# Kernel tuning notes

Measured on AMD Instinct MI355X. Metric: run time of the kernel, lower is better.

## Reference

```python
import jax, jax.numpy as jnp
import numpy as np

D_MODEL, D_EDGE, D_STRUCT = 128, 64, 8
N, E, B = 50000, 800000, 1

def _lin(key, din, dout):
    kw, kb = jax.random.split(key)
    s = 1.0 / np.sqrt(din)
    return (jax.random.uniform(kw, (din, dout), jnp.float32, -s, s),
            jax.random.uniform(kb, (dout,), jnp.float32, -s, s))

def setup_inputs() -> dict:
    key = jax.random.key(0)
    ks = jax.random.split(key, 16)
    H = jax.random.normal(ks[0], (B, N, D_MODEL), jnp.float32)
    xyz = jax.random.normal(ks[1], (B, N, 3), jnp.float32)
    edge_index = jax.random.randint(ks[2], (2, E), 0, N, jnp.int64)
    edge_struct = jax.random.normal(ks[3], (E, D_STRUCT), jnp.float32)
    edge_rest_lengths = jax.random.uniform(ks[4], (E,), jnp.float32)
    We1, be1 = _lin(ks[5], 2 * D_MODEL + 2 + D_STRUCT, D_EDGE)
    We2, be2 = _lin(ks[6], D_EDGE, D_EDGE)
    Wg1, bg1 = _lin(ks[7], 2 + D_STRUCT, 32)
    Wg2, bg2 = _lin(ks[8], 32, 1)
    Wn1, bn1 = _lin(ks[9], D_MODEL + D_EDGE, 2 * D_MODEL)
    Wn2, bn2 = _lin(ks[10], 2 * D_MODEL, D_MODEL)
    ln_g = jnp.ones((D_MODEL,), jnp.float32)
    ln_b = jnp.zeros((D_MODEL,), jnp.float32)
    return dict(H=H, xyz=xyz, edge_index=edge_index, edge_struct=edge_struct,
                edge_rest_lengths=edge_rest_lengths,
                We1=We1, be1=be1, We2=We2, be2=be2,
                Wg1=Wg1, bg1=bg1, Wg2=Wg2, bg2=bg2,
                Wn1=Wn1, bn1=bn1, Wn2=Wn2, bn2=bn2,
                ln_g=ln_g, ln_b=ln_b)

def reference(H, xyz, edge_index, edge_struct, edge_rest_lengths,
              We1, be1, We2, be2, Wg1, bg1, Wg2, bg2,
              Wn1, bn1, Wn2, bn2, ln_g, ln_b):
    Bn, Nn, d = H.shape
    i, j = edge_index[0], edge_index[1]
    # edge geometry
    diff = xyz[:, i, :] - xyz[:, j, :]                      # (B,E,3)
    dist2 = jnp.sum(diff * diff, axis=-1, keepdims=True)    # (B,E,1)
    dist = jnp.sqrt(dist2 + 1e-9)
    rest = edge_rest_lengths.reshape(1, -1, 1)
    delta = (dist - rest) / (rest + 1e-9)
    struct = jnp.broadcast_to(edge_struct[None], (Bn, edge_struct.shape[0], edge_struct.shape[1]))
    # edge message MLP
    Hi, Hj = H[:, i, :], H[:, j, :]
    e_in = jnp.concatenate([Hi, Hj, dist2, delta, struct], axis=-1)  # (B,E,2d+2+ds)
    e = jax.nn.silu(e_in @ We1 + be1)
    e_msg = jax.nn.silu(e @ We2 + be2)                       # (B,E,d_edge)
    # gate
    g_in = jnp.concatenate([dist2, delta, struct], axis=-1)
    g = jax.nn.sigmoid(jax.nn.silu(g_in @ Wg1 + bg1) @ Wg2 + bg2)  # (B,E,1)
    e_msg = e_msg * g
    # scatter-add aggregate to destination node i
    agg = jnp.zeros((Bn, Nn, e_msg.shape[-1]), H.dtype).at[:, i, :].add(e_msg)
    # node MLP (dropout is identity at eval) + residual + LayerNorm
    n_in = jnp.concatenate([H, agg], axis=-1)
    upd = jax.nn.silu(n_in @ Wn1 + bn1) @ Wn2 + bn2
    x = H + upd
    mu = jnp.mean(x, axis=-1, keepdims=True)
    var = jnp.mean((x - mu) ** 2, axis=-1, keepdims=True)
    return (x - mu) / jnp.sqrt(var + 1e-5) * ln_g + ln_b
```

## Files before the change

kernel.cpp:

```cpp
#include <hip/hip_runtime.h>
#include <stdint.h>

#define N_NODES 50000
#define N_EDGES 800000
#define NODE_TILES 782

#define SE   72
#define SW2  72
#define SPQ  136
#define SN1  216
#define SN2  280
#define ATS  40
#define MSTR 72

#define EC_GRID 962
#define EC_CHUNK 13

#define SCAN_B 98

#define FP_PQ_BLOCKS 256
#define FP_GRID 2048
#define FP_FILL_STRIDE ((FP_GRID - FP_PQ_BLOCKS) * 256)

typedef short bf16x8 __attribute__((ext_vector_type(8)));
typedef short short4v __attribute__((ext_vector_type(4)));
typedef unsigned short ushort8 __attribute__((ext_vector_type(8)));
typedef float f32x4  __attribute__((ext_vector_type(4)));

static __device__ __forceinline__ unsigned short f2bf(float f) {
  unsigned int x = __float_as_uint(f);
  unsigned int r = (x + 0x7fffu + ((x >> 16) & 1u)) >> 16;
  return (unsigned short)r;
}
static __device__ __forceinline__ float bf2f(unsigned short u) {
  return __uint_as_float(((unsigned int)u) << 16);
}
static __device__ __forceinline__ float silu_f(float x) {
  return x * __builtin_amdgcn_rcpf(1.0f + __expf(-x));
}
static __device__ __forceinline__ float sigmoid_f(float x) {
  return __builtin_amdgcn_rcpf(1.0f + __expf(-x));
}
static __device__ __forceinline__ unsigned int cvt_pk_bf16(float lo, float hi) {
  unsigned int r;
  asm("v_cvt_pk_bf16_f32 %0, %1, %2" : "=v"(r) : "v"(lo), "v"(hi));
  return r;
}
static __device__ __forceinline__ bf16x8 pack8(float4 u, float4 v) {
  bf16x8 w;
  w[0] = (short)f2bf(u.x); w[1] = (short)f2bf(u.y);
  w[2] = (short)f2bf(u.z); w[3] = (short)f2bf(u.w);
  w[4] = (short)f2bf(v.x); w[5] = (short)f2bf(v.y);
  w[6] = (short)f2bf(v.z); w[7] = (short)f2bf(v.w);
  return w;
}

__global__ void prep_hist(
    const int* __restrict__ eidx,
    const float* __restrict__ We1, const float* __restrict__ be1,
    const float* __restrict__ We2,
    const float* __restrict__ Wn1, const float* __restrict__ Wn2,
    unsigned short* __restrict__ WpqT, unsigned short* __restrict__ We2T,
    unsigned short* __restrict__ Wn1T, unsigned short* __restrict__ Wn2T,
    unsigned short* __restrict__ WrT,
    int* __restrict__ cnt)
{
  const int gid = blockIdx.x * 256 + threadIdx.x;
  const int gsz = gridDim.x * 256;
  for (int i = gid; i < 128 * SPQ; i += gsz) {
    int n = i / SPQ, k = i % SPQ;
    unsigned short v = 0;
    if (k < 128) v = (n < 64) ? f2bf(We1[k * 64 + n]) : f2bf(We1[(128 + k) * 64 + (n - 64)]);
    WpqT[i] = v;
  }
  for (int i = gid; i < 64 * SW2; i += gsz) {
    int n = i / SW2, k = i % SW2;
    We2T[i] = (k < 64) ? f2bf(We2[k * 64 + n]) : (unsigned short)0;
  }
  for (int i = gid; i < 256 * SN1; i += gsz) {
    int n = i / SN1, k = i % SN1;
    Wn1T[i] = (k < 192) ? f2bf(Wn1[k * 256 + n]) : (unsigned short)0;
  }
  for (int i = gid; i < 128 * SN2; i += gsz) {
    int n = i / SN2, k = i % SN2;
    Wn2T[i] = (k < 256) ? f2bf(Wn2[k * 128 + n]) : (unsigned short)0;
  }
  for (int i = gid; i < 64 * 32; i += gsz) {
    int n = i >> 5, k = i & 31;
    float v = 0.f;
    if (k < 2)       v = We1[256 * 64 + n];
    else if (k < 4)  v = We1[257 * 64 + n];
    else if (k < 12) v = We1[(258 + (k - 4)) * 64 + n];
    else if (k == 12) v = be1[n];
    else if (k == 13) { float w = We1[256 * 64 + n]; v = w - bf2f(f2bf(w)); }
    else if (k == 14) { float w = We1[257 * 64 + n]; v = w - bf2f(f2bf(w)); }
    else if (k == 15) { float w = be1[n];            v = w - bf2f(f2bf(w)); }
    WrT[i] = (k < 16) ? f2bf(v) : (unsigned short)0;
  }
  if (gid < N_EDGES) atomicAdd(&cnt[eidx[gid]], 1);
}

__global__ __launch_bounds__(512) void scan_local(
    const int* __restrict__ cnt, int* __restrict__ rowptr,
    int* __restrict__ bsum)
{
  __shared__ int wsum[8], woff[8];
  const int t = threadIdx.x;
  const int idx = blockIdx.x * 512 + t;
  const int lane = t & 63, wid = t >> 6;
  int c = (idx < N_NODES) ? cnt[idx] : 0;
  int v = c;
  #pragma unroll
  for (int o = 1; o < 64; o <<= 1) {
    int u = __shfl_up(v, o);
    if (lane >= o) v += u;
  }
  if (lane == 63) wsum[wid] = v;
  __syncthreads();
  if (t == 0) {
    int a = 0;
    #pragma unroll
    for (int w = 0; w < 8; ++w) { woff[w] = a; a += wsum[w]; }
    bsum[blockIdx.x] = a;
  }
  __syncthreads();
  if (idx < N_NODES) rowptr[idx] = woff[wid] + (v - c);
}

__global__ __launch_bounds__(128) void scan_mid(
    const int* __restrict__ bsum, int* __restrict__ boff)
{
  __shared__ int ws[2];
  const int t = threadIdx.x;
  const int lane = t & 63, wid = t >> 6;
  int c = (t < SCAN_B) ? bsum[t] : 0;
  int v = c;
  #pragma unroll
  for (int o = 1; o < 64; o <<= 1) {
    int u = __shfl_up(v, o);
    if (lane >= o) v += u;
  }
  if (lane == 63) ws[wid] = v;
  __syncthreads();
  int add = (wid == 1) ? ws[0] : 0;
  if (t < SCAN_B) boff[t] = add + (v - c);
}

__global__ __launch_bounds__(512) void scan_add(
    const int* __restrict__ rowptr, const int* __restrict__ boff,
    int* __restrict__ cursor, float4* __restrict__ agg)
{
  const int idx = blockIdx.x * 512 + threadIdx.x;
  if (idx < N_NODES) cursor[idx] = rowptr[idx] + boff[blockIdx.x];
  if (idx < 50048) {
    float4 z = make_float4(0.f, 0.f, 0.f, 0.f);
    float4* p = agg + (long)idx * 16;
    #pragma unroll
    for (int k = 0; k < 16; ++k) p[k] = z;
  }
}

__global__ __launch_bounds__(256, 3) void fill_pq(
    const float* __restrict__ H, const unsigned short* __restrict__ WpqT,
    unsigned short* __restrict__ P, unsigned short* __restrict__ Q,
    unsigned short* __restrict__ Hbf,
    const int* __restrict__ eidx, const float* __restrict__ xyz,
    const float* __restrict__ estruct, const float* __restrict__ erest,
    int* __restrict__ cursor,
    const float* __restrict__ Wg1, const float* __restrict__ bg1,
    const float* __restrict__ Wg2, const float* __restrict__ bg2,
    unsigned short* __restrict__ rec)
{
  __shared__ unsigned short As[64 * SPQ];
  __shared__ unsigned short Ws[128 * SPQ];

  const int bid = blockIdx.x;
  const int tid = threadIdx.x;

  if (bid < FP_PQ_BLOCKS) {
    const int lane = tid & 63;
    const int wv   = tid >> 6;
    const int lr   = lane & 15;
    const int lq   = lane >> 4;
    const int m0   = wv * 16;

    for (int i = tid * 8; i < 128 * SPQ; i += 256 * 8)
      *(bf16x8*)&Ws[i] = *(const bf16x8*)&WpqT[i];

    f32x4 zero4 = {0.f, 0.f, 0.f, 0.f};
    for (int t = bid; t < NODE_TILES; t += FP_PQ_BLOCKS) {
      const int n0 = t * 64;
      __syncthreads();
      {
        int le = tid >> 2, q = tid & 3;
        int node = n0 + le; if (node >= N_NODES) node = N_NODES - 1;
        const float* src = H + (long)node * 128 + q * 32;
        unsigned short* dst = &As[le * SPQ + q * 32];
        #pragma unroll
        for (int c = 0; c < 32; c += 8) {
          float4 u = *(const float4*)(src + c);
          float4 v = *(const float4*)(src + c + 4);
          *(bf16x8*)(dst + c) = pack8(u, v);
        }
      }
      __syncthreads();

      for (int idx = tid * 8; idx < 64 * 128; idx += 256 * 8) {
        int row = idx >> 7, col = idx & 127;
        *(bf16x8*)&Hbf[((long)n0 + row) * 128 + col] = *(const bf16x8*)&As[row * SPQ + col];
      }

      f32x4 acc[8];
      #pragma unroll
      for (int f = 0; f < 8; ++f) acc[f] = zero4;
      #pragma unroll
      for (int s = 0; s < 4; ++s) {
        int kb = s * 32 + lq * 8;
        bf16x8 a = *(const bf16x8*)&As[(m0 + lr) * SPQ + kb];
        #pragma unroll
        for (int f = 0; f < 8; ++f) {
          bf16x8 b = *(const bf16x8*)&Ws[(f * 16 + lr) * SPQ + kb];
          acc[f] = __builtin_amdgcn_mfma_f32_16x16x32_bf16(a, b, acc[f], 0, 0, 0);
        }
      }
      #pragma unroll
      for (int f = 0; f < 8; ++f) {
        #pragma unroll
        for (int r = 0; r < 4; ++r) {
          int node = n0 + m0 + lq * 4 + r;
          if (node < N_NODES) {
            if (f < 4) P[(long)node * 64 + f * 16 + lr] = f2bf(acc[f][r]);
            else       Q[(long)node * 64 + (f - 4) * 16 + lr] = f2bf(acc[f][r]);
          }
        }
      }
    }
  } else {
    for (int e = (bid - FP_PQ_BLOCKS) * 256 + tid; e < N_EDGES; e += FP_FILL_STRIDE) {
      int i = eidx[e], j = eidx[N_EDGES + e];
      float dx = xyz[i * 3 + 0] - xyz[j * 3 + 0];
      float dy = xyz[i * 3 + 1] - xyz[j * 3 + 1];
      float dz = xyz[i * 3 + 2] - xyz[j * 3 + 2];
      float d2 = dx * dx + dy * dy + dz * dz;
      float dist = sqrtf(d2 + 1e-9f);
      float rest = erest[e];
      float dl = (dist - rest) / (rest + 1e-9f);
      float4 s0 = *(const float4*)&estruct[e * 8];
      float4 s1 = *(const float4*)&estruct[e * 8 + 4];
      float st[8] = {s0.x, s0.y, s0.z, s0.w, s1.x, s1.y, s1.z, s1.w};
      float gsum = 0.f;
      #pragma unroll
      for (int h = 0; h < 32; ++h) {
        float a = bg1[h] + d2 * Wg1[0 * 32 + h] + dl * Wg1[1 * 32 + h];
        #pragma unroll
        for (int c = 0; c < 8; ++c) a += st[c] * Wg1[(2 + c) * 32 + h];
        gsum += silu_f(a) * Wg2[h];
      }
      float g = sigmoid_f(gsum + bg2[0]);

      unsigned short d2h = f2bf(d2);
      unsigned short d2l = f2bf(d2 - bf2f(d2h));
      unsigned short dlh = f2bf(dl);
      unsigned short dll = f2bf(dl - bf2f(dlh));

      ushort8 w0;
      w0[0] = d2h; w0[1] = d2l; w0[2] = dlh; w0[3] = dll;
      w0[4] = f2bf(st[0]); w0[5] = f2bf(st[1]); w0[6] = f2bf(st[2]); w0[7] = f2bf(st[3]);
      uint4 w1;
      w1.x = (unsigned int)f2bf(st[4]) | ((unsigned int)f2bf(st[5]) << 16);
      w1.y = (unsigned int)f2bf(st[6]) | ((unsigned int)f2bf(st[7]) << 16);
      w1.z = __float_as_uint(g);
      w1.w = (unsigned int)i | ((unsigned int)j << 16);

      int pos = atomicAdd(&cursor[i], 1);
      unsigned short* dst = rec + (long)pos * 16;
      *(ushort8*)dst = w0;
      *(uint4*)(dst + 8) = w1;
    }
  }
}

__global__ __launch_bounds__(256, 4) void edge_compute(
    const unsigned short* __restrict__ P, const unsigned short* __restrict__ Q,
    const unsigned short* __restrict__ rec,
    const unsigned short* __restrict__ We2T, const float* __restrict__ be2,
    const unsigned short* __restrict__ WrT,
    float* __restrict__ agg)
{
  __shared__ unsigned short W2s[64 * SW2];
  __shared__ unsigned short Es [4 * 16 * SE];
  __shared__ unsigned short At [4 * 16 * ATS];
  __shared__ unsigned short Ms [4 * 16 * MSTR];

  const int tid  = threadIdx.x;
  const int lane = tid & 63;
  const int wv   = tid >> 6;
  const int lr   = lane & 15;
  const int lq   = lane >> 4;

  for (int i = tid * 8; i < 64 * SW2; i += 256 * 8)
    *(bf16x8*)&W2s[i] = *(const bf16x8*)&We2T[i];

  unsigned short* Es_w = &Es[wv * 16 * SE];
  unsigned short* At_w = &At[wv * 16 * ATS];
  unsigned short* Ms_w = &Ms[wv * 16 * MSTR];

  if (lane < 16) {
    ushort8 z;
    #pragma unroll
    for (int c = 0; c < 8; ++c) z[c] = 0;
    *(ushort8*)&At_w[lane * ATS + 16] = z;
    *(ushort8*)&At_w[lane * ATS + 24] = z;
  }

  bf16x8 aWr[4];
  float bias2[4][4];
  #pragma unroll
  for (int f = 0; f < 4; ++f) {
    aWr[f] = *(const bf16x8*)&WrT[(f * 16 + lr) * 32 + lq * 8];
    #pragma unroll
    for (int r = 0; r < 4; ++r) bias2[f][r] = be2[f * 16 + lq * 4 + r];
  }
  __syncthreads();

  const int n_tiles = N_EDGES / 16;
  const int wid = blockIdx.x * 4 + wv;
  const int t0 = wid * EC_CHUNK;
  const int t1 = (t0 + EC_CHUNK < n_tiles) ? (t0 + EC_CHUNK) : n_tiles;
  if (t0 >= n_tiles) return;

  f32x4 zero4 = {0.f, 0.f, 0.f, 0.f};
  int   cur_node;
  {
    int ij0 = *(const int*)(rec + (long)t0 * 16 * 16 + 14);
    cur_node = ij0 & 0xffff;
  }
  float acc        = 0.f;
  bool  use_atomic = true;

  for (int tile = t0; tile < t1; ++tile) {
    const int s0 = tile * 16;

    const unsigned short* rp = rec + (long)(s0 + lr) * 16;
    ushort8 ra = *(const ushort8*)rp;
    uint4   rb = *(const uint4*)(rp + 8);
    float g     = __uint_as_float(rb.z);
    int   inode = (int)(rb.w & 0xffff);
    int   jnode = (int)((rb.w >> 16) & 0xffff);

    if (lane < 16) {
      ushort8 w1;
      w1[0] = (unsigned short)(rb.x & 0xffff);
      w1[1] = (unsigned short)(rb.x >> 16);
      w1[2] = (unsigned short)(rb.y & 0xffff);
      w1[3] = (unsigned short)(rb.y >> 16);
      w1[4] = 0x3F80u; w1[5] = (unsigned short)ra[0];
      w1[6] = (unsigned short)ra[2]; w1[7] = 0x3F80u;
      *(ushort8*)&At_w[lane * ATS]     = ra;
      *(ushort8*)&At_w[lane * ATS + 8] = w1;
    }

    bf16x8 bA = *(const bf16x8*)&At_w[lr * ATS + lq * 8];
    f32x4 acc1[4];
    #pragma unroll
    for (int f = 0; f < 4; ++f)
      acc1[f] = __builtin_amdgcn_mfma_f32_16x16x32_bf16(aWr[f], bA, zero4, 0, 0, 0);

    const unsigned short* Pb = P + (long)inode * 64;
    const unsigned short* Qb = Q + (long)jnode * 64;
    #pragma unroll
    for (int f = 0; f < 4; ++f) {
      short4v pv = *(const short4v*)&Pb[f * 16 + lq * 4];
      short4v qv = *(const short4v*)&Qb[f * 16 + lq * 4];
      float v0 = silu_f(bf2f((unsigned short)pv[0]) + bf2f((unsigned short)qv[0]) + acc1[f][0]);
      float v1 = silu_f(bf2f((unsigned short)pv[1]) + bf2f((unsigned short)qv[1]) + acc1[f][1]);
      float v2 = silu_f(bf2f((unsigned short)pv[2]) + bf2f((unsigned short)qv[2]) + acc1[f][2]);
      float v3 = silu_f(bf2f((unsigned short)pv[3]) + bf2f((unsigned short)qv[3]) + acc1[f][3]);
      uint2 w;
      w.x = cvt_pk_bf16(v0, v1);
      w.y = cvt_pk_bf16(v2, v3);
      *(uint2*)&Es_w[lr * SE + f * 16 + lq * 4] = w;
    }

    f32x4 acc2[4];
    #pragma unroll
    for (int f = 0; f < 4; ++f) acc2[f] = zero4;
    #pragma unroll
    for (int s = 0; s < 2; ++s) {
      int kb = s * 32 + lq * 8;
      bf16x8 bE = *(const bf16x8*)&Es_w[lr * SE + kb];
      #pragma unroll
      for (int f = 0; f < 4; ++f) {
        bf16x8 aW = *(const bf16x8*)&W2s[(f * 16 + lr) * SW2 + kb];
        acc2[f] = __builtin_amdgcn_mfma_f32_16x16x32_bf16(aW, bE, acc2[f], 0, 0, 0);
      }
    }

    #pragma unroll
    for (int f = 0; f < 4; ++f) {
      float o0 = silu_f(acc2[f][0] + bias2[f][0]) * g;
      float o1 = silu_f(acc2[f][1] + bias2[f][1]) * g;
      float o2 = silu_f(acc2[f][2] + bias2[f][2]) * g;
      float o3 = silu_f(acc2[f][3] + bias2[f][3]) * g;
      uint2 w;
      w.x = cvt_pk_bf16(o0, o1);
      w.y = cvt_pk_bf16(o2, o3);
      *(uint2*)&Ms_w[lr * MSTR + f * 16 + lq * 4] = w;
    }

    float mv[16];
    #pragma unroll
    for (int e = 0; e < 16; ++e) mv[e] = bf2f(Ms_w[e * MSTR + lane]);

    int up = __shfl_up(inode, 1);
    unsigned long long bm = __ballot(inode != up);
    unsigned mask = (unsigned)bm & 0xFFFEu;
    int i0 = __builtin_amdgcn_readlane(inode, 0);
    if (i0 != cur_node) mask |= 1u;

    #pragma unroll
    for (int e = 0; e < 16; ++e) {
      if (mask & (1u << e)) {
        if (use_atomic) atomicAdd(&agg[(long)cur_node * 64 + lane], acc);
        else            agg[(long)cur_node * 64 + lane] = acc;
        use_atomic = false;
        cur_node = __builtin_amdgcn_readlane(inode, e);
        acc = 0.f;
      }
      acc += mv[e];
    }
  }
  atomicAdd(&agg[(long)cur_node * 64 + lane], acc);
}

__global__ __launch_bounds__(256, 2) void h1_kernel(
    const unsigned short* __restrict__ Hbf, const float* __restrict__ agg,
    const unsigned short* __restrict__ Wn1T, const float* __restrict__ bn1,
    unsigned short* __restrict__ h1)
{
  __shared__ unsigned short Wl[128 * SN1];

  const int tid  = threadIdx.x;
  const int lane = tid & 63;
  const int wv   = tid >> 6;
  const int lr   = lane & 15;
  const int lq   = lane >> 4;
  const int m0   = wv * 16;
  const int p    = blockIdx.x & 1;

  for (int i = tid * 8; i < 128 * SN1; i += 256 * 8)
    *(bf16x8*)&Wl[i] = *(const bf16x8*)&Wn1T[p * 128 * SN1 + i];
  __syncthreads();

  f32x4 zero4 = {0.f, 0.f, 0.f, 0.f};
  for (int t = blockIdx.x >> 1; t < NODE_TILES; t += 256) {
    const int n0 = t * 64;
    int rowa = n0 + m0 + lr;
    int rowc = rowa < N_NODES ? rowa : N_NODES - 1;

    f32x4 acc1[8];
    #pragma unroll
    for (int f = 0; f < 8; ++f) acc1[f] = zero4;
    #pragma unroll
    for (int s = 0; s < 6; ++s) {
      int kb = s * 32 + lq * 8;
      bf16x8 a;
      if (s < 4) {
        a = *(const bf16x8*)&Hbf[(long)rowa * 128 + kb];
      } else {
        const float* pp = agg + (long)rowc * 64 + (kb - 128);
        float4 u = *(const float4*)pp;
        float4 v = *(const float4*)(pp + 4);
        a = pack8(u, v);
      }
      #pragma unroll
      for (int f = 0; f < 8; ++f) {
        bf16x8 b = *(const bf16x8*)&Wl[(f * 16 + lr) * SN1 + kb];
        acc1[f] = __builtin_amdgcn_mfma_f32_16x16x32_bf16(a, b, acc1[f], 0, 0, 0);
      }
    }
    #pragma unroll
    for (int f = 0; f < 8; ++f) {
      int col = p * 128 + f * 16 + lr;
      float bias = bn1[col];
      #pragma unroll
      for (int r = 0; r < 4; ++r) {
        int node = n0 + m0 + lq * 4 + r;
        h1[(long)node * 256 + col] = f2bf(silu_f(acc1[f][r] + bias));
      }
    }
  }
}

__global__ __launch_bounds__(256, 2) void out_kernel(
    const float* __restrict__ H, const unsigned short* __restrict__ h1,
    const unsigned short* __restrict__ Wn2T, const float* __restrict__ bn2,
    const float* __restrict__ ln_g, const float* __restrict__ ln_b,
    float* __restrict__ out)
{
  __shared__ unsigned short Wl[128 * SN2];

  const int tid  = threadIdx.x;
  const int lane = tid & 63;
  const int wv   = tid >> 6;
  const int lr   = lane & 15;
  const int lq   = lane >> 4;
  const int m0   = wv * 16;

  for (int i = tid * 8; i < 128 * SN2; i += 256 * 8)
    *(bf16x8*)&Wl[i] = *(const bf16x8*)&Wn2T[i];
  __syncthreads();

  f32x4 zero4 = {0.f, 0.f, 0.f, 0.f};
  for (int t = blockIdx.x; t < NODE_TILES; t += 512) {
    const int n0 = t * 64;
    int rowa = n0 + m0 + lr;

    f32x4 acc2[8];
    #pragma unroll
    for (int f = 0; f < 8; ++f) acc2[f] = zero4;
    #pragma unroll
    for (int s = 0; s < 8; ++s) {
      int kb = s * 32 + lq * 8;
      bf16x8 a = *(const bf16x8*)&h1[(long)rowa * 256 + kb];
      #pragma unroll
      for (int f = 0; f < 8; ++f) {
        bf16x8 b = *(const bf16x8*)&Wl[(f * 16 + lr) * SN2 + kb];
        acc2[f] = __builtin_amdgcn_mfma_f32_16x16x32_bf16(a, b, acc2[f], 0, 0, 0);
      }
    }

    #pragma unroll
    for (int r = 0; r < 4; ++r) {
      int node = n0 + m0 + lq * 4 + r;
      int nc = node < N_NODES ? node : N_NODES - 1;
      float x[8];
      float sum = 0.f, sumsq = 0.f;
      #pragma unroll
      for (int f = 0; f < 8; ++f) {
        int n = f * 16 + lr;
        float u = acc2[f][r] + bn2[n];
        float xv = H[(long)nc * 128 + n] + u;
        x[f] = xv;
        sum += xv;
        sumsq += xv * xv;
      }
      #pragma unroll
      for (int o = 1; o < 16; o <<= 1) {
        sum   += __shfl_xor(sum, o);
        sumsq += __shfl_xor(sumsq, o);
      }
      float mu  = sum * (1.f / 128.f);
      float var = sumsq * (1.f / 128.f) - mu * mu;
      float rstd = rsqrtf(var + 1e-5f);
      if (node < N_NODES) {
        #pragma unroll
        for (int f = 0; f < 8; ++f) {
          int n = f * 16 + lr;
          out[(long)node * 128 + n] = (x[f] - mu) * rstd * ln_g[n] + ln_b[n];
        }
      }
    }
  }
}

extern "C" void kernel_launch(void* const* d_in, const int* in_sizes, int n_in,
                              void* d_out, int out_size, void* d_ws, size_t ws_size,
                              hipStream_t stream) {
  const float* H       = (const float*)d_in[0];
  const float* xyz     = (const float*)d_in[1];
  const int*   eidx    = (const int*)d_in[2];
  const float* estruct = (const float*)d_in[3];
  const float* erest   = (const float*)d_in[4];
  const float* We1     = (const float*)d_in[5];
  const float* be1     = (const float*)d_in[6];
  const float* We2     = (const float*)d_in[7];
  const float* be2     = (const float*)d_in[8];
  const float* Wg1     = (const float*)d_in[9];
  const float* bg1     = (const float*)d_in[10];
  const float* Wg2     = (const float*)d_in[11];
  const float* bg2     = (const float*)d_in[12];
  const float* Wn1     = (const float*)d_in[13];
  const float* bn1     = (const float*)d_in[14];
  const float* Wn2     = (const float*)d_in[15];
  const float* bn2     = (const float*)d_in[16];
  const float* ln_g    = (const float*)d_in[17];
  const float* ln_b    = (const float*)d_in[18];

  char* ws = (char*)d_ws;
  float*          agg    = (float*)(ws + 0);
  unsigned short* Hbf    = (unsigned short*)(ws + 12812288);
  unsigned short* rec    = (unsigned short*)(ws + 25624576);
  unsigned short* P      = (unsigned short*)(ws + 51224576);
  unsigned short* Qm     = (unsigned short*)(ws + 57624576);
  int*            cnt    = (int*)(ws + 64024576);
  int*            rowptr = (int*)(ws + 64224768);
  int*            cursor = (int*)(ws + 64424960);
  unsigned short* WpqT   = (unsigned short*)(ws + 64625152);
  unsigned short* We2T   = (unsigned short*)(ws + 64659968);
  unsigned short* Wn1T   = (unsigned short*)(ws + 64669184);
  unsigned short* Wn2T   = (unsigned short*)(ws + 64779776);
  unsigned short* WrT    = (unsigned short*)(ws + 64851456);
  int*            bsum   = (int*)(ws + 64855552);
  int*            boff   = (int*)(ws + 64856064);
  unsigned short* h1     = (unsigned short*)(ws + 64856576);
  float* out = (float*)d_out;

  hipMemsetAsync(cnt, 0, (size_t)N_NODES * sizeof(int), stream);

  hipLaunchKernelGGL(prep_hist, dim3(3125), dim3(256), 0, stream,
                     eidx, We1, be1, We2, Wn1, Wn2, WpqT, We2T, Wn1T, Wn2T, WrT, cnt);
  hipLaunchKernelGGL(scan_local, dim3(SCAN_B), dim3(512), 0, stream,
                     cnt, rowptr, bsum);
  hipLaunchKernelGGL(scan_mid, dim3(1), dim3(128), 0, stream,
                     bsum, boff);
  hipLaunchKernelGGL(scan_add, dim3(SCAN_B), dim3(512), 0, stream,
                     rowptr, boff, cursor, (float4*)agg);
  hipLaunchKernelGGL(fill_pq, dim3(FP_GRID), dim3(256), 0, stream,
                     H, WpqT, P, Qm, Hbf,
                     eidx, xyz, estruct, erest, cursor,
                     Wg1, bg1, Wg2, bg2, rec);
  hipLaunchKernelGGL(edge_compute, dim3(EC_GRID), dim3(256), 0, stream,
                     P, Qm, rec, We2T, be2, WrT, agg);
  hipLaunchKernelGGL(h1_kernel, dim3(512), dim3(256), 0, stream,
                     Hbf, agg, Wn1T, bn1, h1);
  hipLaunchKernelGGL(out_kernel, dim3(512), dim3(256), 0, stream,
                     H, h1, Wn2T, bn2, ln_g, ln_b, out);
}
```

Before: 381.0 us.

## Split fill_pq work by wave instead of by block, load H directly to registers

Rather than dedicating whole blocks to either the node projection GEMM or the edge fill, every block now gives two waves a 64-node tile (each wave covering 32 rows) and the other two waves the edge loop. The As staging buffer and its syncs are removed: H rows are read from global memory, packed to bf16 in registers, written to Hbf and fed straight into the MFMAs. The grid shrinks to 1024 blocks and launch bounds allow 4 blocks per SM to raise occupancy. The aim is to overlap GEMM and edge work inside each CU and cut LDS traffic. In exchange, every block now loads the full weight tile into LDS, and the global H reads are less coalesced.

```diff
diff --git a/kernel.cpp b/kernel.cpp
--- a/kernel.cpp
+++ b/kernel.cpp
@@ -18,9 +18,7 @@
 
 #define SCAN_B 98
 
-#define FP_PQ_BLOCKS 256
-#define FP_GRID 2048
-#define FP_FILL_STRIDE ((FP_GRID - FP_PQ_BLOCKS) * 256)
+#define FP_GRID 1024
 
 typedef short bf16x8 __attribute__((ext_vector_type(8)));
 typedef short short4v __attribute__((ext_vector_type(4)));
@@ -160,7 +158,7 @@
   }
 }
 
-__global__ __launch_bounds__(256, 3) void fill_pq(
+__global__ __launch_bounds__(256, 4) void fill_pq(
     const float* __restrict__ H, const unsigned short* __restrict__ WpqT,
     unsigned short* __restrict__ P, unsigned short* __restrict__ Q,
     unsigned short* __restrict__ Hbf,
@@ -171,72 +169,67 @@
     const float* __restrict__ Wg2, const float* __restrict__ bg2,
     unsigned short* __restrict__ rec)
 {
-  __shared__ unsigned short As[64 * SPQ];
   __shared__ unsigned short Ws[128 * SPQ];
 
   const int bid = blockIdx.x;
   const int tid = threadIdx.x;
-
-  if (bid < FP_PQ_BLOCKS) {
-    const int lane = tid & 63;
-    const int wv   = tid >> 6;
-    const int lr   = lane & 15;
-    const int lq   = lane >> 4;
-    const int m0   = wv * 16;
-
-    for (int i = tid * 8; i < 128 * SPQ; i += 256 * 8)
-      *(bf16x8*)&Ws[i] = *(const bf16x8*)&WpqT[i];
-
-    f32x4 zero4 = {0.f, 0.f, 0.f, 0.f};
-    for (int t = bid; t < NODE_TILES; t += FP_PQ_BLOCKS) {
-      const int n0 = t * 64;
-      __syncthreads();
-      {
-        int le = tid >> 2, q = tid & 3;
-        int node = n0 + le; if (node >= N_NODES) node = N_NODES - 1;
-        const float* src = H + (long)node * 128 + q * 32;
-        unsigned short* dst = &As[le * SPQ + q * 32];
+  const int wv  = tid >> 6;
+
+  for (int i = tid * 8; i < 128 * SPQ; i += 256 * 8)
+    *(bf16x8*)&Ws[i] = *(const bf16x8*)&WpqT[i];
+  __syncthreads();
+
+  if (wv < 2) {
+    if (bid < NODE_TILES) {
+      const int lane = tid & 63;
+      const int lr   = lane & 15;
+      const int lq   = lane >> 4;
+      const int n0   = bid * 64;
+      const int m0   = wv * 32;
+
+      f32x4 zero4 = {0.f, 0.f, 0.f, 0.f};
+      f32x4 acc[2][8];
+      #pragma unroll
+      for (int h = 0; h < 2; ++h)
         #pragma unroll
-        for (int c = 0; c < 32; c += 8) {
-          float4 u = *(const float4*)(src + c);
-          float4 v = *(const float4*)(src + c + 4);
-          *(bf16x8*)(dst + c) = pack8(u, v);
-        }
-      }
-      __syncthreads();
-
-      for (int idx = tid * 8; idx < 64 * 128; idx += 256 * 8) {
-        int row = idx >> 7, col = idx & 127;
-        *(bf16x8*)&Hbf[((long)n0 + row) * 128 + col] = *(const bf16x8*)&As[row * SPQ + col];
-      }
-
-      f32x4 acc[8];
-      #pragma unroll
-      for (int f = 0; f < 8; ++f) acc[f] = zero4;
+        for (int f = 0; f < 8; ++f) acc[h][f] = zero4;
+
       #pragma unroll
       for (int s = 0; s < 4; ++s) {
         int kb = s * 32 + lq * 8;
-        bf16x8 a = *(const bf16x8*)&As[(m0 + lr) * SPQ + kb];
+        #pragma unroll
+        for (int h = 0; h < 2; ++h) {
+          int rowa = n0 + m0 + h * 16 + lr;
+          int rowc = rowa < N_NODES ? rowa : N_NODES - 1;
+          const float* p = H + (long)rowc * 128 + kb;
+          float4 u = *(const float4*)p;
+          float4 v = *(const float4*)(p + 4);
+          bf16x8 a = pack8(u, v);
+          *(bf16x8*)&Hbf[(long)rowa * 128 + kb] = a;
+          #pragma unroll
+          for (int f = 0; f < 8; ++f) {
+            bf16x8 b = *(const bf16x8*)&Ws[(f * 16 + lr) * SPQ + kb];
+            acc[h][f] = __builtin_amdgcn_mfma_f32_16x16x32_bf16(a, b, acc[h][f], 0, 0, 0);
+          }
+        }
+      }
+      #pragma unroll
+      for (int h = 0; h < 2; ++h) {
         #pragma unroll
         for (int f = 0; f < 8; ++f) {
-          bf16x8 b = *(const bf16x8*)&Ws[(f * 16 + lr) * SPQ + kb];
-          acc[f] = __builtin_amdgcn_mfma_f32_16x16x32_bf16(a, b, acc[f], 0, 0, 0);
-        }
-      }
-      #pragma unroll
-      for (int f = 0; f < 8; ++f) {
-        #pragma unroll
-        for (int r = 0; r < 4; ++r) {
-          int node = n0 + m0 + lq * 4 + r;
-          if (node < N_NODES) {
-            if (f < 4) P[(long)node * 64 + f * 16 + lr] = f2bf(acc[f][r]);
-            else       Q[(long)node * 64 + (f - 4) * 16 + lr] = f2bf(acc[f][r]);
+          #pragma unroll
+          for (int r = 0; r < 4; ++r) {
+            int node = n0 + m0 + h * 16 + lq * 4 + r;
+            if (node < N_NODES) {
+              if (f < 4) P[(long)node * 64 + f * 16 + lr] = f2bf(acc[h][f][r]);
+              else       Q[(long)node * 64 + (f - 4) * 16 + lr] = f2bf(acc[h][f][r]);
+            }
           }
         }
       }
     }
   } else {
-    for (int e = (bid - FP_PQ_BLOCKS) * 256 + tid; e < N_EDGES; e += FP_FILL_STRIDE) {
+    for (int e = bid * 128 + (tid - 128); e < N_EDGES; e += FP_GRID * 128) {
       int i = eidx[e], j = eidx[N_EDGES + e];
       float dx = xyz[i * 3 + 0] - xyz[j * 3 + 0];
       float dy = xyz[i * 3 + 1] - xyz[j * 3 + 1];
```

Result: no change. 381.2 us (+0.0%).

## Split fused fill/PQ kernel into separate edge-fill and node-GEMM launches

Applied to the files above, without the earlier changes.

Replaces the block-specialized fill_pq kernel, which gave some blocks the node projection and the rest a grid-stride edge fill, with two kernels. One runs one thread per edge for geometry, gate and reorder, and the other runs one block per 64-node tile for the projection. The projection now loads H rows straight into registers as MFMA A operands instead of staging them through shared memory. This removes load imbalance and the shared-memory staging, but loses the overlap of the two phases and adds a kernel launch.

```diff
diff --git a/kernel.cpp b/kernel.cpp
--- a/kernel.cpp
+++ b/kernel.cpp
@@ -17,10 +17,6 @@
 #define EC_CHUNK 13
 
 #define SCAN_B 98
-
-#define FP_PQ_BLOCKS 256
-#define FP_GRID 2048
-#define FP_FILL_STRIDE ((FP_GRID - FP_PQ_BLOCKS) * 256)
 
 typedef short bf16x8 __attribute__((ext_vector_type(8)));
 typedef short short4v __attribute__((ext_vector_type(4)));
@@ -160,10 +156,7 @@
   }
 }
 
-__global__ __launch_bounds__(256, 3) void fill_pq(
-    const float* __restrict__ H, const unsigned short* __restrict__ WpqT,
-    unsigned short* __restrict__ P, unsigned short* __restrict__ Q,
-    unsigned short* __restrict__ Hbf,
+__global__ void fill_reorder(
     const int* __restrict__ eidx, const float* __restrict__ xyz,
     const float* __restrict__ estruct, const float* __restrict__ erest,
     int* __restrict__ cursor,
@@ -171,111 +164,99 @@
     const float* __restrict__ Wg2, const float* __restrict__ bg2,
     unsigned short* __restrict__ rec)
 {
-  __shared__ unsigned short As[64 * SPQ];
+  int e = blockIdx.x * 256 + threadIdx.x;
+  if (e >= N_EDGES) return;
+  int i = eidx[e], j = eidx[N_EDGES + e];
+  float dx = xyz[i * 3 + 0] - xyz[j * 3 + 0];
+  float dy = xyz[i * 3 + 1] - xyz[j * 3 + 1];
+  float dz = xyz[i * 3 + 2] - xyz[j * 3 + 2];
+  float d2 = dx * dx + dy * dy + dz * dz;
+  float dist = sqrtf(d2 + 1e-9f);
+  float rest = erest[e];
+  float dl = (dist - rest) / (rest + 1e-9f);
+  float4 s0 = *(const float4*)&estruct[e * 8];
+  float4 s1 = *(const float4*)&estruct[e * 8 + 4];
+  float st[8] = {s0.x, s0.y, s0.z, s0.w, s1.x, s1.y, s1.z, s1.w};
+  float gsum = 0.f;
+  #pragma unroll
+  for (int h = 0; h < 32; ++h) {
+    float a = bg1[h] + d2 * Wg1[0 * 32 + h] + dl * Wg1[1 * 32 + h];
+    #pragma unroll
+    for (int c = 0; c < 8; ++c) a += st[c] * Wg1[(2 + c) * 32 + h];
+    gsum += silu_f(a) * Wg2[h];
+  }
+  float g = sigmoid_f(gsum + bg2[0]);
+
+  unsigned short d2h = f2bf(d2);
+  unsigned short d2l = f2bf(d2 - bf2f(d2h));
+  unsigned short dlh = f2bf(dl);
+  unsigned short dll = f2bf(dl - bf2f(dlh));
+
+  ushort8 w0;
+  w0[0] = d2h; w0[1] = d2l; w0[2] = dlh; w0[3] = dll;
+  w0[4] = f2bf(st[0]); w0[5] = f2bf(st[1]); w0[6] = f2bf(st[2]); w0[7] = f2bf(st[3]);
+  uint4 w1;
+  w1.x = (unsigned int)f2bf(st[4]) | ((unsigned int)f2bf(st[5]) << 16);
+  w1.y = (unsigned int)f2bf(st[6]) | ((unsigned int)f2bf(st[7]) << 16);
+  w1.z = __float_as_uint(g);
+  w1.w = (unsigned int)i | ((unsigned int)j << 16);
+
+  int pos = atomicAdd(&cursor[i], 1);
+  unsigned short* dst = rec + (long)pos * 16;
+  *(ushort8*)dst = w0;
+  *(uint4*)(dst + 8) = w1;
+}
+
+__global__ __launch_bounds__(256, 4) void pq_kernel(
+    const float* __restrict__ H, const unsigned short* __restrict__ WpqT,
+    unsigned short* __restrict__ P, unsigned short* __restrict__ Q,
+    unsigned short* __restrict__ Hbf)
+{
   __shared__ unsigned short Ws[128 * SPQ];
 
-  const int bid = blockIdx.x;
-  const int tid = threadIdx.x;
-
-  if (bid < FP_PQ_BLOCKS) {
-    const int lane = tid & 63;
-    const int wv   = tid >> 6;
-    const int lr   = lane & 15;
-    const int lq   = lane >> 4;
-    const int m0   = wv * 16;
-
-    for (int i = tid * 8; i < 128 * SPQ; i += 256 * 8)
-      *(bf16x8*)&Ws[i] = *(const bf16x8*)&WpqT[i];
-
-    f32x4 zero4 = {0.f, 0.f, 0.f, 0.f};
-    for (int t = bid; t < NODE_TILES; t += FP_PQ_BLOCKS) {
-      const int n0 = t * 64;
-      __syncthreads();
-      {
-        int le = tid >> 2, q = tid & 3;
-        int node = n0 + le; if (node >= N_NODES) node = N_NODES - 1;
-        const float* src = H + (long)node * 128 + q * 32;
-        unsigned short* dst = &As[le * SPQ + q * 32];
-        #pragma unroll
-        for (int c = 0; c < 32; c += 8) {
-          float4 u = *(const float4*)(src + c);
-          float4 v = *(const float4*)(src + c + 4);
-          *(bf16x8*)(dst + c) = pack8(u, v);
-        }
-      }
-      __syncthreads();
-
-      for (int idx = tid * 8; idx < 64 * 128; idx += 256 * 8) {
-        int row = idx >> 7, col = idx & 127;
-        *(bf16x8*)&Hbf[((long)n0 + row) * 128 + col] = *(const bf16x8*)&As[row * SPQ + col];
-      }
-
-      f32x4 acc[8];
-      #pragma unroll
-      for (int f = 0; f < 8; ++f) acc[f] = zero4;
-      #pragma unroll
-      for (int s = 0; s < 4; ++s) {
-        int kb = s * 32 + lq * 8;
-        bf16x8 a = *(const bf16x8*)&As[(m0 + lr) * SPQ + kb];
-        #pragma unroll
-        for (int f = 0; f < 8; ++f) {
-          bf16x8 b = *(const bf16x8*)&Ws[(f * 16 + lr) * SPQ + kb];
-          acc[f] = __builtin_amdgcn_mfma_f32_16x16x32_bf16(a, b, acc[f], 0, 0, 0);
-        }
-      }
-      #pragma unroll
-      for (int f = 0; f < 8; ++f) {
-        #pragma unroll
-        for (int r = 0; r < 4; ++r) {
-          int node = n0 + m0 + lq * 4 + r;
-          if (node < N_NODES) {
-            if (f < 4) P[(long)node * 64 + f * 16 + lr] = f2bf(acc[f][r]);
-            else       Q[(long)node * 64 + (f - 4) * 16 + lr] = f2bf(acc[f][r]);
-          }
-        }
-      }
-    }
-  } else {
-    for (int e = (bid - FP_PQ_BLOCKS) * 256 + tid; e < N_EDGES; e += FP_FILL_STRIDE) {
-      int i = eidx[e], j = eidx[N_EDGES + e];
-      float dx = xyz[i * 3 + 0] - xyz[j * 3 + 0];
-      float dy = xyz[i * 3 + 1] - xyz[j * 3 + 1];
-      float dz = xyz[i * 3 + 2] - xyz[j * 3 + 2];
-      float d2 = dx * dx + dy * dy + dz * dz;
-      float dist = sqrtf(d2 + 1e-9f);
-      float rest = erest[e];
-      float dl = (dist - rest) / (rest + 1e-9f);
-      float4 s0 = *(const float4*)&estruct[e * 8];
-      float4 s1 = *(const float4*)&estruct[e * 8 + 4];
-      float st[8] = {s0.x, s0.y, s0.z, s0.w, s1.x, s1.y, s1.z, s1.w};
-      float gsum = 0.f;
-      #pragma unroll
-      for (int h = 0; h < 32; ++h) {
-        float a = bg1[h] + d2 * Wg1[0 * 32 + h] + dl * Wg1[1 * 32 + h];
-        #pragma unroll
-        for (int c = 0; c < 8; ++c) a += st[c] * Wg1[(2 + c) * 32 + h];
-        gsum += silu_f(a) * Wg2[h];
-      }
-      float g = sigmoid_f(gsum + bg2[0]);
-
-      unsigned short d2h = f2bf(d2);
-      unsigned short d2l = f2bf(d2 - bf2f(d2h));
-      unsigned short dlh = f2bf(dl);
-      unsigned short dll = f2bf(dl - bf2f(dlh));
-
-      ushort8 w0;
-      w0[0] = d2h; w0[1] = d2l; w0[2] = dlh; w0[3] = dll;
-      w0[4] = f2bf(st[0]); w0[5] = f2bf(st[1]); w0[6] = f2bf(st[2]); w0[7] = f2bf(st[3]);
-      uint4 w1;
-      w1.x = (unsigned int)f2bf(st[4]) | ((unsigned int)f2bf(st[5]) << 16);
-      w1.y = (unsigned int)f2bf(st[6]) | ((unsigned int)f2bf(st[7]) << 16);
-      w1.z = __float_as_uint(g);
-      w1.w = (unsigned int)i | ((unsigned int)j << 16);
-
-      int pos = atomicAdd(&cursor[i], 1);
-      unsigned short* dst = rec + (long)pos * 16;
-      *(ushort8*)dst = w0;
-      *(uint4*)(dst + 8) = w1;
+  const int tid  = threadIdx.x;
+  const int lane = tid & 63;
+  const int wv   = tid >> 6;
+  const int lr   = lane & 15;
+  const int lq   = lane >> 4;
+  const int n0   = blockIdx.x * 64;
+  const int m0   = wv * 16;
+
+  for (int i = tid * 8; i < 128 * SPQ; i += 256 * 8)
+    *(bf16x8*)&Ws[i] = *(const bf16x8*)&WpqT[i];
+  __syncthreads();
+
+  const int rowa = n0 + m0 + lr;
+  const int rowc = rowa < N_NODES ? rowa : N_NODES - 1;
+
+  f32x4 zero4 = {0.f, 0.f, 0.f, 0.f};
+  f32x4 acc[8];
+  #pragma unroll
+  for (int f = 0; f < 8; ++f) acc[f] = zero4;
+
+  #pragma unroll
+  for (int s = 0; s < 4; ++s) {
+    int kb = s * 32 + lq * 8;
+    const float* p = H + (long)rowc * 128 + kb;
+    float4 u = *(const float4*)p;
+    float4 v = *(const float4*)(p + 4);
+    bf16x8 a = pack8(u, v);
+    *(bf16x8*)&Hbf[(long)rowa * 128 + kb] = a;
+    #pragma unroll
+    for (int f = 0; f < 8; ++f) {
+      bf16x8 b = *(const bf16x8*)&Ws[(f * 16 + lr) * SPQ + kb];
+      acc[f] = __builtin_amdgcn_mfma_f32_16x16x32_bf16(a, b, acc[f], 0, 0, 0);
+    }
+  }
+  #pragma unroll
+  for (int f = 0; f < 8; ++f) {
+    #pragma unroll
+    for (int r = 0; r < 4; ++r) {
+      int node = n0 + m0 + lq * 4 + r;
+      if (node < N_NODES) {
+        if (f < 4) P[(long)node * 64 + f * 16 + lr] = f2bf(acc[f][r]);
+        else       Q[(long)node * 64 + (f - 4) * 16 + lr] = f2bf(acc[f][r]);
+      }
     }
   }
 }
@@ -616,10 +597,11 @@
                      bsum, boff);
   hipLaunchKernelGGL(scan_add, dim3(SCAN_B), dim3(512), 0, stream,
                      rowptr, boff, cursor, (float4*)agg);
-  hipLaunchKernelGGL(fill_pq, dim3(FP_GRID), dim3(256), 0, stream,
-                     H, WpqT, P, Qm, Hbf,
+  hipLaunchKernelGGL(fill_reorder, dim3(3125), dim3(256), 0, stream,
                      eidx, xyz, estruct, erest, cursor,
                      Wg1, bg1, Wg2, bg2, rec);
+  hipLaunchKernelGGL(pq_kernel, dim3(NODE_TILES), dim3(256), 0, stream,
+                     H, WpqT, P, Qm, Hbf);
   hipLaunchKernelGGL(edge_compute, dim3(EC_GRID), dim3(256), 0, stream,
                      P, Qm, rec, We2T, be2, WrT, agg);
   hipLaunchKernelGGL(h1_kernel, dim3(512), dim3(256), 0, stream,
```

Measured after the change: 363.0 us. 1.05x faster.
